# Kernel optimization log

Hardware: AMD Instinct MI355X
Metric: run time of the kernel (lower is better)

Reference implementation:

```python
import jax, jax.numpy as jnp
import numpy as np

N, E, IN, HID, H, C, NL, OUT = 50000, 500000, 384, 128, 8, 16, 3, 16
NEG_SLOPE = 0.2

def setup_inputs() -> dict:
    key = jax.random.key(0)
    ks = jax.random.split(key, 16)
    s = 0.1
    return {
        "x": jax.random.normal(ks[0], (N, IN), jnp.float32),
        "edge_index": jax.random.randint(ks[1], (2, E), 0, N, jnp.int32),
        "proj_w": jax.random.normal(ks[2], (IN, HID), jnp.float32) * s,
        "proj_b": jax.random.normal(ks[3], (HID,), jnp.float32) * s,
        "lin_w": jax.random.normal(ks[4], (NL, HID, HID), jnp.float32) * s,
        "att_src": jax.random.normal(ks[5], (NL, H, C), jnp.float32) * s,
        "att_dst": jax.random.normal(ks[6], (NL, H, C), jnp.float32) * s,
        "gat_b": jax.random.normal(ks[7], (NL, HID), jnp.float32) * s,
        "ln_g": jnp.ones((NL, HID), jnp.float32),
        "ln_b": jnp.zeros((NL, HID), jnp.float32),
        "cls_w1": jax.random.normal(ks[8], (HID, HID // 2), jnp.float32) * s,
        "cls_b1": jax.random.normal(ks[9], (HID // 2,), jnp.float32) * s,
        "cls_w2": jax.random.normal(ks[10], (HID // 2, OUT), jnp.float32) * s,
        "cls_b2": jax.random.normal(ks[11], (OUT,), jnp.float32) * s,
    }

def _layernorm(h, g, b, eps=1e-5):
    mu = jnp.mean(h, axis=-1, keepdims=True)
    var = jnp.var(h, axis=-1, keepdims=True)
    return (h - mu) * jax.lax.rsqrt(var + eps) * g + b

def _gat_layer(h, src, dst, w, a_src, a_dst, bias):
    # h: [N, HID]; per-head transform -> [N, H, C]
    xh = (h @ w).reshape(N, H, C)
    al_s = jnp.einsum('nhc,hc->nh', xh, a_src)   # [N, H]
    al_d = jnp.einsum('nhc,hc->nh', xh, a_dst)
    e = jax.nn.leaky_relu(al_s[src] + al_d[dst], NEG_SLOPE)  # [E+N, H]
    # segment softmax over incoming edges of each dst node
    m = jax.ops.segment_max(e, dst, num_segments=N)
    e = jnp.exp(e - m[dst])
    denom = jax.ops.segment_sum(e, dst, num_segments=N)
    alpha = e / (denom[dst] + 1e-16)
    msg = xh[src] * alpha[:, :, None]            # [E+N, H, C]
    out = jax.ops.segment_sum(msg, dst, num_segments=N)
    return out.reshape(N, H * C) + bias

def reference(x, edge_index, proj_w, proj_b, lin_w, att_src, att_dst, gat_b,
              ln_g, ln_b, cls_w1, cls_b1, cls_w2, cls_b2):
    loops = jnp.arange(N, dtype=edge_index.dtype)  # PyG GATConv adds self-loops
    src = jnp.concatenate([edge_index[0], loops])
    dst = jnp.concatenate([edge_index[1], loops])
    h = jax.nn.relu(x @ proj_w + proj_b)
    for l in range(NL):
        h_res = h
        h = _gat_layer(h, src, dst, lin_w[l], att_src[l], att_dst[l], gat_b[l])
        h = h + h_res
        h = jax.nn.relu(_layernorm(h, ln_g[l], ln_b[l]))
    logits = jax.nn.relu(h @ cls_w1 + cls_b1) @ cls_w2 + cls_b2
    return jax.nn.log_softmax(logits, axis=1)
```

## Files before the change

### kernel.cpp

```cpp
#include <hip/hip_runtime.h>
#include <hip/hip_bf16.h>
#include <math.h>

#define NN 50000
#define EE 500000
#define DIN 384
#define HIDD 128
#define NHEAD 8
#define OUTD 16

typedef __attribute__((ext_vector_type(8))) __bf16 bf16x8;
typedef __attribute__((ext_vector_type(4))) float f32x4;

__device__ __forceinline__ ushort f2bf(float f) {
  union { float f; unsigned u; } v; v.f = f;
  unsigned r = v.u + 0x7fffu + ((v.u >> 16) & 1u);
  return (ushort)(r >> 16);
}
__device__ __forceinline__ float bflo(unsigned w) {
  union { unsigned u; float f; } v; v.u = w << 16; return v.f;
}
__device__ __forceinline__ float bfhi(unsigned w) {
  union { unsigned u; float f; } v; v.u = w & 0xffff0000u; return v.f;
}
__device__ __forceinline__ bf16x8 pack8(const float4& a, const float4& b) {
  union { bf16x8 v; ushort u[8]; } r;
  r.u[0] = f2bf(a.x); r.u[1] = f2bf(a.y); r.u[2] = f2bf(a.z); r.u[3] = f2bf(a.w);
  r.u[4] = f2bf(b.x); r.u[5] = f2bf(b.y); r.u[6] = f2bf(b.z); r.u[7] = f2bf(b.w);
  return r.v;
}

__global__ void zero_ints(int* p, int n) {
  int i = blockIdx.x * blockDim.x + threadIdx.x;
  if (i < n) p[i] = 0;
}

__global__ void hist_kernel(const int* __restrict__ dst, int* __restrict__ counts, int e) {
  int i = blockIdx.x * blockDim.x + threadIdx.x;
  if (i < e) atomicAdd(&counts[dst[i]], 1);
}

#define SCAN_BS 256
#define SCAN_NBLK ((NN + SCAN_BS - 1) / SCAN_BS)

__global__ __launch_bounds__(256) void partial_sums(const int* __restrict__ counts,
                                                    int* __restrict__ bsum, int n) {
  __shared__ int red[256];
  int i = blockIdx.x * 256 + threadIdx.x;
  red[threadIdx.x] = (i < n) ? counts[i] : 0;
  __syncthreads();
  #pragma unroll
  for (int off = 128; off; off >>= 1) {
    if (threadIdx.x < off) red[threadIdx.x] += red[threadIdx.x + off];
    __syncthreads();
  }
  if (threadIdx.x == 0) bsum[blockIdx.x] = red[0];
}

__global__ __launch_bounds__(256) void scan_bsums(const int* __restrict__ bsum,
                                                  int* __restrict__ boff, int nb) {
  __shared__ int buf[256];
  int t = threadIdx.x;
  int v = (t < nb) ? bsum[t] : 0;
  buf[t] = v;
  __syncthreads();
  #pragma unroll
  for (int off = 1; off < 256; off <<= 1) {
    int u = (t >= off) ? buf[t - off] : 0;
    __syncthreads();
    buf[t] += u;
    __syncthreads();
  }
  if (t < nb) boff[t] = buf[t] - v;
}

__global__ __launch_bounds__(256) void final_scan(const int* __restrict__ counts,
                                                  const int* __restrict__ boff,
                                                  int* __restrict__ rowptr,
                                                  int* __restrict__ woff, int n) {
  __shared__ int buf[256];
  int i = blockIdx.x * 256 + threadIdx.x;
  int t = threadIdx.x;
  int v = (i < n) ? counts[i] : 0;
  buf[t] = v;
  __syncthreads();
  #pragma unroll
  for (int off = 1; off < 256; off <<= 1) {
    int u = (t >= off) ? buf[t - off] : 0;
    __syncthreads();
    buf[t] += u;
    __syncthreads();
  }
  int excl = boff[blockIdx.x] + buf[t] - v;
  if (i < n) { rowptr[i] = excl; woff[i] = excl; }
  if (i == n - 1) rowptr[n] = excl + v;
}

__global__ void scatter_kernel(const int* __restrict__ src, const int* __restrict__ dst,
                               int* __restrict__ woff, int* __restrict__ col, int e) {
  int i = blockIdx.x * blockDim.x + threadIdx.x;
  if (i < e) {
    int p = atomicAdd(&woff[dst[i]], 1);
    col[p] = src[i];
  }
}

__global__ void prep_weights(const float* __restrict__ proj_w,
                             const float* __restrict__ lin_w,
                             const float* __restrict__ cls_w1,
                             const float* __restrict__ cls_w2,
                             ushort* __restrict__ wt) {
  int i = blockIdx.x * blockDim.x + threadIdx.x;
  if (i < 49152) {
    int k = i >> 7, n = i & 127;
    wt[n * 384 + k] = f2bf(proj_w[i]);
  } else if (i < 98304) {
    int j = i - 49152;
    int l = j >> 14, rem = j & 16383;
    int k = rem >> 7, n = rem & 127;
    wt[49152 + l * 16384 + n * 128 + k] = f2bf(lin_w[j]);
  } else if (i < 106496) {
    int j = i - 98304;
    int n = j >> 7, k = j & 127;
    wt[98304 + n * 128 + k] = f2bf(cls_w1[k * 64 + n]);
  } else if (i < 107520) {
    int j = i - 106496;
    int n = j >> 6, k = j & 63;
    wt[106496 + n * 64 + k] = f2bf(cls_w2[k * 16 + n]);
  }
}

#define LDS_STRIDE 72
template<typename AT, int KK, bool RELU_BIAS, bool ATT>
__global__ __launch_bounds__(256) void mfma_gemm64(const AT* __restrict__ A,
                                                   const ushort* __restrict__ Bt,
                                                   const float* __restrict__ bias,
                                                   ushort* __restrict__ C,
                                                   const float* __restrict__ att_s,
                                                   const float* __restrict__ att_d,
                                                   float* __restrict__ al_s,
                                                   float* __restrict__ al_d,
                                                   int M) {
  constexpr int NIT = KK / 64;
  constexpr bool F32A = (sizeof(AT) == 4);
  __shared__ ushort sB[2][128 * LDS_STRIDE];
  const int tid = threadIdx.x;
  const int wave = tid >> 6, lane = tid & 63;
  const int q = lane >> 4, lm = lane & 15;
  const int wr = wave >> 1, wc = wave & 1;
  const int m0 = blockIdx.x * 64;

  int br[4], bc[4];
  #pragma unroll
  for (int p = 0; p < 4; ++p) {
    int idx = p * 256 + tid;
    br[p] = idx >> 3;
    bc[p] = (idx & 7) << 3;
  }

  const float* ap0f = nullptr; const float* ap1f = nullptr;
  const ushort* ap0h = nullptr; const ushort* ap1h = nullptr;
  {
    int r0 = min(m0 + wr * 32 + lm, M - 1);
    int r1 = min(m0 + wr * 32 + 16 + lm, M - 1);
    if constexpr (F32A) {
      ap0f = (const float*)A + (size_t)r0 * KK + q * 8;
      ap1f = (const float*)A + (size_t)r1 * KK + q * 8;
    } else {
      ap0h = (const ushort*)A + (size_t)r0 * KK + q * 8;
      ap1h = (const ushort*)A + (size_t)r1 * KK + q * 8;
    }
  }

  f32x4 acc[2][4];
  #pragma unroll
  for (int i = 0; i < 2; i++)
    #pragma unroll
    for (int j = 0; j < 4; j++) acc[i][j] = {0.f, 0.f, 0.f, 0.f};

  bf16x8 breg[2][4];
  float4 af32[2][2][4];
  bf16x8 abf[2][2][2];

  auto loadB = [&](int buf, int k0) {
    #pragma unroll
    for (int p = 0; p < 4; ++p)
      breg[buf][p] = *(const bf16x8*)(Bt + (size_t)br[p] * KK + k0 + bc[p]);
  };
  auto writeB = [&](int buf) {
    #pragma unroll
    for (int p = 0; p < 4; ++p)
      *(bf16x8*)&sB[buf][br[p] * LDS_STRIDE + bc[p]] = breg[buf][p];
  };
  auto loadA = [&](int buf, int k0) {
    if constexpr (F32A) {
      #pragma unroll
      for (int ks = 0; ks < 2; ++ks) {
        af32[buf][0][ks * 2]     = *(const float4*)(ap0f + k0 + ks * 32);
        af32[buf][0][ks * 2 + 1] = *(const float4*)(ap0f + k0 + ks * 32 + 4);
        af32[buf][1][ks * 2]     = *(const float4*)(ap1f + k0 + ks * 32);
        af32[buf][1][ks * 2 + 1] = *(const float4*)(ap1f + k0 + ks * 32 + 4);
      }
    } else {
      #pragma unroll
      for (int ks = 0; ks < 2; ++ks) {
        abf[buf][0][ks] = *(const bf16x8*)(ap0h + k0 + ks * 32);
        abf[buf][1][ks] = *(const bf16x8*)(ap1h + k0 + ks * 32);
      }
    }
  };
  auto compute = [&](int buf) {
    #pragma unroll
    for (int ks = 0; ks < 2; ++ks) {
      bf16x8 af[2], bfv[4];
      #pragma unroll
      for (int t = 0; t < 2; ++t) {
        if constexpr (F32A)
          af[t] = pack8(af32[buf][t][ks * 2], af32[buf][t][ks * 2 + 1]);
        else
          af[t] = abf[buf][t][ks];
      }
      #pragma unroll
      for (int t = 0; t < 4; ++t)
        bfv[t] = *(const bf16x8*)&sB[buf][(wc * 64 + t * 16 + lm) * LDS_STRIDE + ks * 32 + q * 8];
      #pragma unroll
      for (int i = 0; i < 2; ++i)
        #pragma unroll
        for (int j = 0; j < 4; ++j)
          acc[i][j] = __builtin_amdgcn_mfma_f32_16x16x32_bf16(af[i], bfv[j], acc[i][j], 0, 0, 0);
    }
  };

  loadB(0, 0);
  loadA(0, 0);
  writeB(0);
  __syncthreads();
  #pragma unroll
  for (int it = 0; it < NIT; ++it) {
    if (it + 1 < NIT) {
      loadB((it + 1) & 1, (it + 1) * 64);
      loadA((it + 1) & 1, (it + 1) * 64);
    }
    compute(it & 1);
    if (it + 1 < NIT) {
      writeB((it + 1) & 1);
      __syncthreads();
    }
  }

  float asw[4], adw[4];
  if constexpr (ATT) {
    #pragma unroll
    for (int j = 0; j < 4; ++j) {
      asw[j] = att_s[(wc * 4 + j) * 16 + lm];
      adw[j] = att_d[(wc * 4 + j) * 16 + lm];
    }
  }
  #pragma unroll
  for (int i = 0; i < 2; ++i) {
    #pragma unroll
    for (int r = 0; r < 4; ++r) {
      int row = m0 + wr * 32 + i * 16 + q * 4 + r;
      if (row < M) {
        #pragma unroll
        for (int j = 0; j < 4; ++j) {
          int colc = wc * 64 + j * 16 + lm;
          float v = acc[i][j][r];
          if (RELU_BIAS) { v += bias[colc]; v = fmaxf(v, 0.f); }
          C[(size_t)row * 128 + colc] = f2bf(v);
        }
      }
    }
  }
  if constexpr (ATT) {
    #pragma unroll
    for (int i = 0; i < 2; ++i) {
      #pragma unroll
      for (int j = 0; j < 4; ++j) {
        #pragma unroll
        for (int r = 0; r < 4; ++r) {
          float ss = acc[i][j][r] * asw[j];
          float dd = acc[i][j][r] * adw[j];
          #pragma unroll
          for (int off = 1; off < 16; off <<= 1) {
            ss += __shfl_xor(ss, off);
            dd += __shfl_xor(dd, off);
          }
          if (lm == 0) {
            int row = m0 + wr * 32 + i * 16 + q * 4 + r;
            if (row < M) {
              al_s[row * 8 + wc * 4 + j] = ss;
              al_d[row * 8 + wc * 4 + j] = dd;
            }
          }
        }
      }
    }
  }
}

__global__ __launch_bounds__(256) void gat_aggregate(
    const ushort* __restrict__ xh, const float* __restrict__ al_s,
    const float* __restrict__ al_d, const int* __restrict__ rowptr,
    const int* __restrict__ col, const ushort* __restrict__ h_res,
    const float* __restrict__ gb, const float* __restrict__ lng,
    const float* __restrict__ lnb, ushort* __restrict__ h_out, int n) {
  const int lane = threadIdx.x & 63;
  const int node = (blockIdx.x * blockDim.x + threadIdx.x) >> 6;
  if (node >= n) return;
  const int e8 = lane >> 3;
  const int hh = lane & 7;
  const int head = lane >> 3;
  const unsigned* xw_base = (const unsigned*)xh;

  const int start = rowptr[node], end = rowptr[node + 1];
  const int T = end - start + 1;
  const float ald_c = al_d[node * 8 + hh];

  float m = -INFINITY, denom = 0.f, acc0 = 0.f, acc1 = 0.f;

  for (int c = 0; c < T; c += 8) {
    int it = c + e8;
    bool valid = it < T;
    int idx = start + it;
    int s = (valid && idx < end) ? col[idx] : node;
    float e = al_s[s * 8 + hh] + ald_c;
    e = (e > 0.f) ? e : 0.2f * e;
    if (!valid) e = -INFINITY;
    float cm = e;
    cm = fmaxf(cm, __shfl_xor(cm, 8));
    cm = fmaxf(cm, __shfl_xor(cm, 16));
    cm = fmaxf(cm, __shfl_xor(cm, 32));
    float newm = fmaxf(m, __shfl(cm, head));
    float newm_c = __shfl(newm, hh * 8);
    float p_lane = __expf(e - newm_c);
    float scale = __expf(m - newm);
    m = newm;
    unsigned xg[8];
    int sj[8];
    #pragma unroll
    for (int j = 0; j < 8; ++j) sj[j] = __shfl(s, j * 8);
    #pragma unroll
    for (int j = 0; j < 8; ++j) xg[j] = xw_base[(size_t)sj[j] * 64 + lane];
    denom *= scale; acc0 *= scale; acc1 *= scale;
    #pragma unroll
    for (int j = 0; j < 8; ++j) {
      float pj = __shfl(p_lane, j * 8 + head);
      denom += pj;
      acc0 = fmaf(pj, bflo(xg[j]), acc0);
      acc1 = fmaf(pj, bfhi(xg[j]), acc1);
    }
  }

  float inv = 1.f / denom;
  int c0 = lane * 2, c1 = c0 + 1;
  unsigned ur = ((const unsigned*)h_res)[(size_t)node * 64 + lane];
  float v0 = acc0 * inv + gb[c0] + bflo(ur);
  float v1 = acc1 * inv + gb[c1] + bfhi(ur);
  float sum = v0 + v1;
  #pragma unroll
  for (int off = 32; off; off >>= 1) sum += __shfl_xor(sum, off);
  float mean = sum * (1.f / 128.f);
  float d0 = v0 - mean, d1 = v1 - mean;
  float sq = d0 * d0 + d1 * d1;
  #pragma unroll
  for (int off = 32; off; off >>= 1) sq += __shfl_xor(sq, off);
  float rstd = rsqrtf(sq * (1.f / 128.f) + 1e-5f);
  float o0 = fmaxf(d0 * rstd * lng[c0] + lnb[c0], 0.f);
  float o1 = fmaxf(d1 * rstd * lng[c1] + lnb[c1], 0.f);
  ((unsigned*)h_out)[(size_t)node * 64 + lane] =
      (unsigned)f2bf(o0) | ((unsigned)f2bf(o1) << 16);
}

#define CSTR 136
#define HSTR 72
__global__ __launch_bounds__(256) void classifier_mfma(
    const ushort* __restrict__ h, const ushort* __restrict__ w1t,
    const float* __restrict__ b1, const ushort* __restrict__ w2t,
    const float* __restrict__ b2, float* __restrict__ out, int n) {
  __shared__ ushort sA[128 * CSTR];
  __shared__ ushort sB[64 * CSTR];
  __shared__ ushort sHid[128 * HSTR];
  const int tid = threadIdx.x;
  const int wave = tid >> 6, lane = tid & 63;
  const int q = lane >> 4, lm = lane & 15;
  const int wr = wave >> 1, wc = wave & 1;
  const int m0 = blockIdx.x * 128;

  #pragma unroll
  for (int p = 0; p < 8; ++p) {
    int idx = p * 256 + tid;
    int r = idx >> 4;
    int c = (idx & 15) << 3;
    int row = min(m0 + r, n - 1);
    *(bf16x8*)&sA[r * CSTR + c] = *(const bf16x8*)(h + (size_t)row * 128 + c);
  }
  #pragma unroll
  for (int p = 0; p < 4; ++p) {
    int idx = p * 256 + tid;
    int r = idx >> 4;
    int c = (idx & 15) << 3;
    *(bf16x8*)&sB[r * CSTR + c] = *(const bf16x8*)(w1t + r * 128 + c);
  }
  __syncthreads();

  f32x4 acc[4][2];
  #pragma unroll
  for (int i = 0; i < 4; ++i)
    #pragma unroll
    for (int j = 0; j < 2; ++j) acc[i][j] = {0.f, 0.f, 0.f, 0.f};
  #pragma unroll
  for (int ks = 0; ks < 4; ++ks) {
    bf16x8 af[4], bfv[2];
    #pragma unroll
    for (int t = 0; t < 4; ++t)
      af[t] = *(const bf16x8*)&sA[(wr * 64 + t * 16 + lm) * CSTR + ks * 32 + q * 8];
    #pragma unroll
    for (int j = 0; j < 2; ++j)
      bfv[j] = *(const bf16x8*)&sB[(wc * 32 + j * 16 + lm) * CSTR + ks * 32 + q * 8];
    #pragma unroll
    for (int i = 0; i < 4; ++i)
      #pragma unroll
      for (int j = 0; j < 2; ++j)
        acc[i][j] = __builtin_amdgcn_mfma_f32_16x16x32_bf16(af[i], bfv[j], acc[i][j], 0, 0, 0);
  }
  #pragma unroll
  for (int i = 0; i < 4; ++i) {
    #pragma unroll
    for (int j = 0; j < 2; ++j) {
      int colc = wc * 32 + j * 16 + lm;
      float bb = b1[colc];
      #pragma unroll
      for (int r = 0; r < 4; ++r) {
        int row = wr * 64 + i * 16 + q * 4 + r;
        float v = fmaxf(acc[i][j][r] + bb, 0.f);
        sHid[row * HSTR + colc] = f2bf(v);
      }
    }
  }
  __syncthreads();

  f32x4 acc2[2] = {{0.f, 0.f, 0.f, 0.f}, {0.f, 0.f, 0.f, 0.f}};
  #pragma unroll
  for (int ks = 0; ks < 2; ++ks) {
    bf16x8 b2f = *(const bf16x8*)(w2t + lm * 64 + ks * 32 + q * 8);
    #pragma unroll
    for (int t = 0; t < 2; ++t) {
      bf16x8 a2 = *(const bf16x8*)&sHid[(wave * 32 + t * 16 + lm) * HSTR + ks * 32 + q * 8];
      acc2[t] = __builtin_amdgcn_mfma_f32_16x16x32_bf16(a2, b2f, acc2[t], 0, 0, 0);
    }
  }
  float bb2 = b2[lm];
  #pragma unroll
  for (int t = 0; t < 2; ++t) {
    #pragma unroll
    for (int r = 0; r < 4; ++r) {
      int row = m0 + wave * 32 + t * 16 + q * 4 + r;
      float lg = acc2[t][r] + bb2;
      float mx = lg;
      #pragma unroll
      for (int off = 8; off; off >>= 1) mx = fmaxf(mx, __shfl_xor(mx, off, 16));
      float se = __expf(lg - mx);
      #pragma unroll
      for (int off = 8; off; off >>= 1) se += __shfl_xor(se, off, 16);
      if (row < n) out[(size_t)row * 16 + lm] = lg - mx - __logf(se);
    }
  }
}

extern "C" void kernel_launch(void* const* d_in, const int* in_sizes, int n_in,
                              void* d_out, int out_size, void* d_ws, size_t ws_size,
                              hipStream_t stream) {
  const float* x       = (const float*)d_in[0];
  const int*   ei      = (const int*)d_in[1];
  const float* proj_w  = (const float*)d_in[2];
  const float* proj_b  = (const float*)d_in[3];
  const float* lin_w   = (const float*)d_in[4];
  const float* att_src = (const float*)d_in[5];
  const float* att_dst = (const float*)d_in[6];
  const float* gat_b   = (const float*)d_in[7];
  const float* ln_g    = (const float*)d_in[8];
  const float* ln_b    = (const float*)d_in[9];
  const float* cls_w1  = (const float*)d_in[10];
  const float* cls_b1  = (const float*)d_in[11];
  const float* cls_w2  = (const float*)d_in[12];
  const float* cls_b2  = (const float*)d_in[13];
  float* outp = (float*)d_out;

  const int N = NN, E = EE;
  ushort* wt   = (ushort*)d_ws;
  ushort* h0   = wt + 108544;
  ushort* h1   = h0 + (size_t)N * 128;
  ushort* xh_u = h1 + (size_t)N * 128;
  float* als   = (float*)(xh_u + (size_t)N * 128);
  float* ald   = als + (size_t)N * NHEAD;
  int* counts  = (int*)(ald + (size_t)N * NHEAD);
  int* rowptr  = counts + N;
  int* woff    = rowptr + N + 1;
  int* col     = woff + N;
  int* bsum    = col + E;
  int* boff    = bsum + SCAN_NBLK;

  const int* e_src = ei;
  const int* e_dst = ei + E;

  prep_weights<<<(107520 + 255) / 256, 256, 0, stream>>>(proj_w, lin_w, cls_w1, cls_w2, wt);

  zero_ints<<<(N + 255) / 256, 256, 0, stream>>>(counts, N);
  hist_kernel<<<(E + 255) / 256, 256, 0, stream>>>(e_dst, counts, E);
  partial_sums<<<SCAN_NBLK, 256, 0, stream>>>(counts, bsum, N);
  scan_bsums<<<1, 256, 0, stream>>>(bsum, boff, SCAN_NBLK);
  final_scan<<<SCAN_NBLK, 256, 0, stream>>>(counts, boff, rowptr, woff, N);
  scatter_kernel<<<(E + 255) / 256, 256, 0, stream>>>(e_src, e_dst, woff, col, E);

  const int gblocks = (N + 63) / 64;
  mfma_gemm64<float, DIN, true, false><<<gblocks, 256, 0, stream>>>(
      x, wt, proj_b, h0, nullptr, nullptr, nullptr, nullptr, N);

  ushort* hc = h0;
  ushort* hn = h1;
  for (int l = 0; l < 3; ++l) {
    mfma_gemm64<ushort, HIDD, false, true><<<gblocks, 256, 0, stream>>>(
        hc, wt + 49152 + l * 16384, nullptr, xh_u,
        att_src + l * 128, att_dst + l * 128, als, ald, N);
    gat_aggregate<<<(N + 3) / 4, 256, 0, stream>>>(
        xh_u, als, ald, rowptr, col, hc, gat_b + l * 128, ln_g + l * 128,
        ln_b + l * 128, hn, N);
    ushort* t = hc; hc = hn; hn = t;
  }
  classifier_mfma<<<(N + 127) / 128, 256, 0, stream>>>(
      hc, wt + 98304, cls_b1, wt + 106496, cls_b2, outp, N);
}
```

Measured before the change: 398.9 us.

## Load GEMM B fragments directly from global memory, dropping LDS staging

The GEMM kernel no longer stages the transposed weight tile through shared memory with barriers. Each lane now loads its MFMA B fragments straight from global memory into double-buffered registers. This removes the LDS writes, LDS reads and __syncthreads per k-step. In exchange, each wave re-reads weights from global memory or cache, which makes redundant global loads across waves and uses more registers.

```diff
diff --git a/kernel.cpp b/kernel.cpp
--- a/kernel.cpp
+++ b/kernel.cpp
@@ -130,7 +130,6 @@
   }
 }
 
-#define LDS_STRIDE 72
 template<typename AT, int KK, bool RELU_BIAS, bool ATT>
 __global__ __launch_bounds__(256) void mfma_gemm64(const AT* __restrict__ A,
                                                    const ushort* __restrict__ Bt,
@@ -143,20 +142,11 @@
                                                    int M) {
   constexpr int NIT = KK / 64;
   constexpr bool F32A = (sizeof(AT) == 4);
-  __shared__ ushort sB[2][128 * LDS_STRIDE];
   const int tid = threadIdx.x;
   const int wave = tid >> 6, lane = tid & 63;
   const int q = lane >> 4, lm = lane & 15;
   const int wr = wave >> 1, wc = wave & 1;
   const int m0 = blockIdx.x * 64;
-
-  int br[4], bc[4];
-  #pragma unroll
-  for (int p = 0; p < 4; ++p) {
-    int idx = p * 256 + tid;
-    br[p] = idx >> 3;
-    bc[p] = (idx & 7) << 3;
-  }
 
   const float* ap0f = nullptr; const float* ap1f = nullptr;
   const ushort* ap0h = nullptr; const ushort* ap1h = nullptr;
@@ -171,6 +161,10 @@
       ap1h = (const ushort*)A + (size_t)r1 * KK + q * 8;
     }
   }
+  const ushort* bp[4];
+  #pragma unroll
+  for (int t = 0; t < 4; ++t)
+    bp[t] = Bt + (size_t)(wc * 64 + t * 16 + lm) * KK + q * 8;
 
   f32x4 acc[2][4];
   #pragma unroll
@@ -178,21 +172,11 @@
     #pragma unroll
     for (int j = 0; j < 4; j++) acc[i][j] = {0.f, 0.f, 0.f, 0.f};
 
-  bf16x8 breg[2][4];
   float4 af32[2][2][4];
   bf16x8 abf[2][2][2];
-
-  auto loadB = [&](int buf, int k0) {
-    #pragma unroll
-    for (int p = 0; p < 4; ++p)
-      breg[buf][p] = *(const bf16x8*)(Bt + (size_t)br[p] * KK + k0 + bc[p]);
-  };
-  auto writeB = [&](int buf) {
-    #pragma unroll
-    for (int p = 0; p < 4; ++p)
-      *(bf16x8*)&sB[buf][br[p] * LDS_STRIDE + bc[p]] = breg[buf][p];
-  };
-  auto loadA = [&](int buf, int k0) {
+  bf16x8 bfrag[2][4][2];
+
+  auto loadStep = [&](int buf, int k0) {
     if constexpr (F32A) {
       #pragma unroll
       for (int ks = 0; ks < 2; ++ks) {
@@ -208,11 +192,16 @@
         abf[buf][1][ks] = *(const bf16x8*)(ap1h + k0 + ks * 32);
       }
     }
+    #pragma unroll
+    for (int t = 0; t < 4; ++t)
+      #pragma unroll
+      for (int ks = 0; ks < 2; ++ks)
+        bfrag[buf][t][ks] = *(const bf16x8*)(bp[t] + k0 + ks * 32);
   };
-  auto compute = [&](int buf) {
+  auto computeStep = [&](int buf) {
     #pragma unroll
     for (int ks = 0; ks < 2; ++ks) {
-      bf16x8 af[2], bfv[4];
+      bf16x8 af[2];
       #pragma unroll
       for (int t = 0; t < 2; ++t) {
         if constexpr (F32A)
@@ -221,31 +210,19 @@
           af[t] = abf[buf][t][ks];
       }
       #pragma unroll
-      for (int t = 0; t < 4; ++t)
-        bfv[t] = *(const bf16x8*)&sB[buf][(wc * 64 + t * 16 + lm) * LDS_STRIDE + ks * 32 + q * 8];
-      #pragma unroll
       for (int i = 0; i < 2; ++i)
         #pragma unroll
         for (int j = 0; j < 4; ++j)
-          acc[i][j] = __builtin_amdgcn_mfma_f32_16x16x32_bf16(af[i], bfv[j], acc[i][j], 0, 0, 0);
+          acc[i][j] = __builtin_amdgcn_mfma_f32_16x16x32_bf16(af[i], bfrag[buf][j][ks],
+                                                              acc[i][j], 0, 0, 0);
     }
   };
 
-  loadB(0, 0);
-  loadA(0, 0);
-  writeB(0);
-  __syncthreads();
+  loadStep(0, 0);
   #pragma unroll
   for (int it = 0; it < NIT; ++it) {
-    if (it + 1 < NIT) {
-      loadB((it + 1) & 1, (it + 1) * 64);
-      loadA((it + 1) & 1, (it + 1) * 64);
-    }
-    compute(it & 1);
-    if (it + 1 < NIT) {
-      writeB((it + 1) & 1);
-      __syncthreads();
-    }
+    if (it + 1 < NIT) loadStep((it + 1) & 1, (it + 1) * 64);
+    computeStep(it & 1);
   }
 
   float asw[4], adw[4];
```

Result: slower. 436.3 us (+9.4%).
